# Performance work log

Hardware: AMD Instinct MI355X
Metric: run time of the kernel (lower is better)

Reference implementation:

```python
import jax, jax.numpy as jnp
import numpy as np

NUM_HEADS = 8
D_HEAD = 64
LN_EPS = 1e-6


def _pad_idx(lengths, max_len):
    # flat indices into a [B*max_len, ...] dense buffer for each packed token
    return np.concatenate([b * max_len + np.arange(int(l)) for b, l in enumerate(lengths)])


def _layer_norm(x, scale, bias):
    mu = jnp.mean(x, axis=-1, keepdims=True)
    var = jnp.mean(jnp.square(x - mu), axis=-1, keepdims=True)
    return (x - mu) * jax.lax.rsqrt(var + LN_EPS) * scale + bias


def setup_inputs() -> dict:
    key = jax.random.key(0)
    ks = jax.random.split(key, 12)
    d_model, d_ff, H, dh = 512, 2048, NUM_HEADS, D_HEAD
    lengths = np.array([128 * (i + 1) for i in range(8)], dtype=np.int64)  # sum = 4608
    total = int(lengths.sum())
    s = 0.02
    return {
        "x": jax.random.normal(ks[0], (total, d_model), jnp.float32),
        "mem": jax.random.normal(ks[1], (total, d_model), jnp.float32),
        "lengths_x": lengths,
        "lengths_mem": lengths.copy(),
        "Wq": jax.random.normal(ks[2], (d_model, H * dh), jnp.float32) * s,
        "Wk": jax.random.normal(ks[3], (d_model, H * dh), jnp.float32) * s,
        "Wv": jax.random.normal(ks[4], (d_model, H * dh), jnp.float32) * s,
        "Wo": jax.random.normal(ks[5], (H * dh, d_model), jnp.float32) * s,
        "ln1_scale": jnp.ones((d_model,), jnp.float32),
        "ln1_bias": jnp.zeros((d_model,), jnp.float32),
        "W1": jax.random.normal(ks[6], (d_model, d_ff), jnp.float32) * s,
        "b1": jnp.zeros((d_ff,), jnp.float32),
        "W2": jax.random.normal(ks[7], (d_ff, d_model), jnp.float32) * s,
        "b2": jnp.zeros((d_model,), jnp.float32),
        "ln2_scale": jnp.ones((d_model,), jnp.float32),
        "ln2_bias": jnp.zeros((d_model,), jnp.float32),
    }


def reference(x, mem, lengths_x, lengths_mem, Wq, Wk, Wv, Wo,
              ln1_scale, ln1_bias, W1, b1, W2, b2, ln2_scale, ln2_bias):
    lx = np.asarray(lengths_x)
    lm = np.asarray(lengths_mem)
    B = lx.shape[0]
    Lx = int(lx.max())
    Lm = int(lm.max())
    H, dh = NUM_HEADS, D_HEAD

    idx_x = _pad_idx(lx, Lx)
    idx_m = _pad_idx(lm, Lm)

    def pad(packed, idx, B, L):
        dense = jnp.zeros((B * L,) + packed.shape[1:], packed.dtype).at[idx].set(packed)
        return dense.reshape((B, L) + packed.shape[1:])

    q = pad((x @ Wq).reshape(-1, H, dh), idx_x, B, Lx)   # [B, Lx, H, dh]
    k = pad((mem @ Wk).reshape(-1, H, dh), idx_m, B, Lm)  # [B, Lm, H, dh]
    v = pad((mem @ Wv).reshape(-1, H, dh), idx_m, B, Lm)

    e = jnp.einsum('bxhd,byhd->bhxy', q, k) / np.sqrt(dh)  # [B, H, Lx, Lm]
    # validity mask: (query pos < len_x) & (key pos < len_mem)
    mask = (np.arange(Lx)[None, :, None] < lx[:, None, None]) & \
           (np.arange(Lm)[None, None, :] < lm[:, None, None])
    mask = jnp.asarray(mask)[:, None, :, :]  # [B, 1, Lx, Lm]
    e = jnp.where(mask, e, jnp.float32(-1e30))  # finite -inf surrogate; identical softmax on valid rows
    alpha = jax.nn.softmax(e, axis=-1)
    out = jnp.einsum('bhxy,byhd->bxhd', alpha, v).reshape(B, Lx, H * dh)
    out = out @ Wo                                  # [B, Lx, d_model]
    out = out.reshape(B * Lx, -1)[idx_x]            # pack back to [total_x, d_model]

    h = _layer_norm(x + out, ln1_scale, ln1_bias)
    ffn = jax.nn.relu(h @ W1 + b1) @ W2 + b2
    return _layer_norm(h + ffn, ln2_scale, ln2_bias)
```

## Files before the change

### kernel.cpp

```cpp
#include <hip/hip_runtime.h>
#include <stdint.h>

typedef short bf8v __attribute__((ext_vector_type(8)));
typedef float f4v  __attribute__((ext_vector_type(4)));
typedef short s8v  __attribute__((ext_vector_type(8)));

__device__ __forceinline__ float bf2f(short b){
  unsigned u = ((unsigned)(unsigned short)b) << 16;
  union { unsigned u; float f; } c; c.u = u; return c.f;
}
__device__ __forceinline__ short f2bf(float f){
  union { float f; unsigned u; } c; c.f = f;
  unsigned r = (c.u + 0x7FFFu + ((c.u >> 16) & 1u)) >> 16;
  return (short)r;
}
__device__ __forceinline__ void gload16(const short* g, short* l){
  __builtin_amdgcn_global_load_lds(
      (const __attribute__((address_space(1))) void*)g,
      (__attribute__((address_space(3))) void*)l, 16, 0, 0);
}

__global__ void prep_kernel(const int* lx, const int* lm, int* meta){
  if (threadIdx.x != 0) return;
  int is64 = ((lx[1] | lx[3] | lx[5] | lx[7]) == 0) ? 1 : 0;
  int ox = 0, om = 0;
  for (int b = 0; b < 8; ++b){
    int a = is64 ? lx[2*b] : lx[b];
    int c = is64 ? lm[2*b] : lm[b];
    meta[b] = a; meta[8+b] = c;
    meta[16+b] = ox; meta[25+b] = om;
    ox += a; om += c;
  }
  meta[24] = ox; meta[33] = om;
}

__global__ __launch_bounds__(256) void cvt2bf(const float* __restrict__ x,
                                              const float* __restrict__ mem,
                                              short* __restrict__ xb,
                                              short* __restrict__ mb,
                                              long long n){
  long long t = (long long)blockIdx.x * 256 + threadIdx.x;
  long long i = t * 8;
  const float* s; short* d;
  if (i < n){ s = x + i; d = xb + i; }
  else {
    i -= n; if (i >= n) return;
    s = mem + i; d = mb + i;
  }
  float4 f0 = *(const float4*)s;
  float4 f1 = *(const float4*)(s + 4);
  s8v o;
  o[0]=f2bf(f0.x); o[1]=f2bf(f0.y); o[2]=f2bf(f0.z); o[3]=f2bf(f0.w);
  o[4]=f2bf(f1.x); o[5]=f2bf(f1.y); o[6]=f2bf(f1.z); o[7]=f2bf(f1.w);
  *(s8v*)d = o;
}

__global__ __launch_bounds__(256) void cvt_w_t(
    const float* __restrict__ Wq, const float* __restrict__ Wk,
    const float* __restrict__ Wv, const float* __restrict__ Wo,
    const float* __restrict__ W1, const float* __restrict__ W2,
    short* __restrict__ WqT, short* __restrict__ WkT,
    short* __restrict__ WvT, short* __restrict__ WoT,
    short* __restrict__ W1T, short* __restrict__ W2T){
  __shared__ float tile[32][33];
  int bid = blockIdx.x;
  const float* W; short* WT; int K, N, t0;
  if      (bid <  256){ W=Wq; WT=WqT; K=512;  N=512;  t0=0;    }
  else if (bid <  512){ W=Wk; WT=WkT; K=512;  N=512;  t0=256;  }
  else if (bid <  768){ W=Wv; WT=WvT; K=512;  N=512;  t0=512;  }
  else if (bid < 1024){ W=Wo; WT=WoT; K=512;  N=512;  t0=768;  }
  else if (bid < 2048){ W=W1; WT=W1T; K=512;  N=2048; t0=1024; }
  else                { W=W2; WT=W2T; K=2048; N=512;  t0=2048; }
  int lt = bid - t0;
  int ntn = N / 32;
  int tk = lt / ntn, tn = lt % ntn;
  int r0 = threadIdx.x >> 5, c = threadIdx.x & 31;
  #pragma unroll
  for (int i = 0; i < 4; ++i){
    int r = r0 + i*8;
    tile[r][c] = W[(long)(tk*32 + r)*N + tn*32 + c];
  }
  __syncthreads();
  #pragma unroll
  for (int i = 0; i < 4; ++i){
    int r = r0 + i*8;
    WT[(long)(tn*32 + r)*K + tk*32 + c] = f2bf(tile[c][r]);
  }
}

template<int BM>
__device__ __forceinline__ void stage_gemm(const short* A, const short* Bt,
    long brow, long bcol, int M, int N, int K, int t,
    short* Als, short* Bls){
  int tid = threadIdx.x;
  #pragma unroll
  for (int i = 0; i < BM/64; ++i){
    int cc = i*256 + tid;
    int row = cc >> 2, slot = cc & 3;
    int cg = slot ^ ((row >> 1) & 3);
    long ar = brow + row; if (ar >= M) ar = M - 1;
    gload16(A + ar*(long)K + t + cg*8, &Als[cc*8]);
  }
  #pragma unroll
  for (int i = 0; i < 2; ++i){
    int cc = i*256 + tid;
    int row = cc >> 2, slot = cc & 3;
    int cg = slot ^ ((row >> 1) & 3);
    long br = bcol + row; if (br >= N) br = N - 1;
    gload16(Bt + br*(long)K + t + cg*8, &Bls[cc*8]);
  }
}

template<int BM>
__device__ __forceinline__ void gemm_core(const short* A, const short* Bt,
    short* __restrict__ C, const float* __restrict__ bias,
    int M, int N, int K, float scale, int relu, int colmajor,
    long brow, long bcol, short* Als, short* Bls){
  constexpr int NREP = (BM == 128) ? 4 : 2;
  int tid = threadIdx.x;
  int lane = tid & 63, w = tid >> 6;
  int wrow = (BM == 128) ? (w >> 1) * 64 : 0;
  int wcol = (BM == 128) ? (w & 1) * 64 : w * 32;
  int l15 = lane & 15, l4 = lane >> 4;

  f4v acc[4][NREP];
  #pragma unroll
  for (int m = 0; m < 4; ++m)
    #pragma unroll
    for (int n = 0; n < NREP; ++n) acc[m][n] = (f4v){0.f,0.f,0.f,0.f};

  int nt = K / 32;
  stage_gemm<BM>(A, Bt, brow, bcol, M, N, K, 0, Als, Bls);
  for (int t = 0; t < nt; ++t){
    __syncthreads();
    if (t + 1 < nt)
      stage_gemm<BM>(A, Bt, brow, bcol, M, N, K, (t+1)*32,
                     Als + ((t+1)&1)*(BM*32), Bls + ((t+1)&1)*4096);
    const short* Ab = Als + (t&1)*(BM*32);
    const short* Bb = Bls + (t&1)*4096;
    bf8v a[4], b[NREP];
    #pragma unroll
    for (int m = 0; m < 4; ++m){
      int row = wrow + m*16 + l15;
      int slot = l4 ^ ((row >> 1) & 3);
      a[m] = *(const bf8v*)&Ab[row*32 + slot*8];
    }
    #pragma unroll
    for (int n = 0; n < NREP; ++n){
      int row = wcol + n*16 + l15;
      int slot = l4 ^ ((row >> 1) & 3);
      b[n] = *(const bf8v*)&Bb[row*32 + slot*8];
    }
    #pragma unroll
    for (int m = 0; m < 4; ++m)
      #pragma unroll
      for (int n = 0; n < NREP; ++n)
        acc[m][n] = __builtin_amdgcn_mfma_f32_16x16x32_bf16(a[m], b[n], acc[m][n], 0, 0, 0);
  }

  #pragma unroll
  for (int m = 0; m < 4; ++m){
    #pragma unroll
    for (int n = 0; n < NREP; ++n){
      long col = bcol + wcol + n*16 + l15;
      float bi = (bias != nullptr && col < N) ? bias[col] : 0.f;
      #pragma unroll
      for (int j = 0; j < 4; ++j){
        long row = brow + wrow + m*16 + 4*l4 + j;
        if (row < M && col < N){
          float v = acc[m][n][j] * scale + bi;
          if (relu) v = fmaxf(v, 0.f);
          C[colmajor ? (col*(long)M + row) : (row*(long)N + col)] = f2bf(v);
        }
      }
    }
  }
}

__global__ __launch_bounds__(256) void gemm_bt(
    const short* __restrict__ A, const short* __restrict__ Bt,
    short* __restrict__ C, const float* __restrict__ bias,
    int M, int N, int K, float scale, int relu, int colmajor){
  __shared__ __align__(16) short Als[2*128*32];
  __shared__ __align__(16) short Bls[2*128*32];
  gemm_core<128>(A, Bt, C, bias, M, N, K, scale, relu, colmajor,
                 (long)blockIdx.y * 128, (long)blockIdx.x * 128, Als, Bls);
}

__global__ __launch_bounds__(256) void gemm_bt64(
    const short* __restrict__ A, const short* __restrict__ Bt,
    short* __restrict__ C, const float* __restrict__ bias,
    int M, int N, int K, float scale, int relu, int colmajor){
  __shared__ __align__(16) short Als[2*64*32];
  __shared__ __align__(16) short Bls[2*128*32];
  gemm_core<64>(A, Bt, C, bias, M, N, K, scale, relu, colmajor,
                (long)blockIdx.y * 64, (long)blockIdx.x * 128, Als, Bls);
}

__global__ __launch_bounds__(256) void gemm_qkv(
    const short* __restrict__ xb, const short* __restrict__ mb,
    const short* __restrict__ WqT, const short* __restrict__ WkT,
    const short* __restrict__ WvT,
    short* __restrict__ Qb, short* __restrict__ Kbf, short* __restrict__ Vtb,
    int total){
  __shared__ __align__(16) short Als[2*64*32];
  __shared__ __align__(16) short Bls[2*128*32];
  int seg = blockIdx.x >> 2;
  const short* A  = (seg == 0) ? xb : mb;
  const short* Bt = (seg == 0) ? WqT : ((seg == 1) ? WkT : WvT);
  short* C        = (seg == 0) ? Qb  : ((seg == 1) ? Kbf : Vtb);
  float scale     = (seg == 0) ? 0.125f : 1.f;
  int colmajor    = (seg == 2);
  gemm_core<64>(A, Bt, C, nullptr, total, 512, 512, scale, 0, colmajor,
                (long)blockIdx.y * 64, (long)(blockIdx.x & 3) * 128, Als, Bls);
}

__global__ __launch_bounds__(512) void attn_kernel(
    const short* __restrict__ Q, const short* __restrict__ Kb,
    const short* __restrict__ Vt, short* __restrict__ Ob,
    const int* __restrict__ meta, int total){
  int qt = blockIdx.x, h = blockIdx.y, b = blockIdx.z;
  int Lx = meta[b], Lm = meta[8+b];
  int ox = meta[16+b], om = meta[25+b];
  if (qt*128 >= Lx) return;

  __shared__ __align__(16) short Kls[3][64*64];
  __shared__ __align__(16) short Vls[3][64*64];
  __shared__ __align__(16) short Pls[8][16*64];

  int tid = threadIdx.x;
  int lane = tid & 63, w = tid >> 6;
  int l15 = lane & 15, l4 = lane >> 4;

  bf8v aq0, aq1;
  {
    int qrow = qt*128 + w*16 + l15;
    int grow = ox + (qrow < Lx ? qrow : Lx - 1);
    const short* qp = Q + (long)grow*512 + h*64 + l4*8;
    aq0 = *(const bf8v*)qp;
    aq1 = *(const bf8v*)(qp + 32);
  }
  float mrun[4] = {-1e30f,-1e30f,-1e30f,-1e30f};
  float lrun[4] = {0.f,0.f,0.f,0.f};
  f4v o[4];
  #pragma unroll
  for (int n = 0; n < 4; ++n) o[n] = (f4v){0.f,0.f,0.f,0.f};

  int nt = (Lm + 63) / 64;

  #define ATTN_STAGE(T, BUF)                                                   \
    {                                                                          \
      int c = tid;                                                             \
      int rr = c >> 3, slot = c & 7;                                           \
      int ch = slot ^ (rr & 7);                                                \
      int kv0_ = (T) * 64;                                                     \
      int tok = kv0_ + rr; if (tok >= Lm) tok = Lm - 1;                        \
      gload16(Kb + (long)(om + tok)*512 + h*64 + ch*8, &Kls[BUF][c*8]);        \
      int kvs = kv0_ + ch*8; if (kvs + 8 > Lm) kvs = Lm - 8;                   \
      gload16(Vt + (long)(h*64 + rr)*total + om + kvs, &Vls[BUF][c*8]);        \
    }

  ATTN_STAGE(0, 0)
  if (1 < nt) ATTN_STAGE(1, 1)

  int buf = 0;
  for (int t = 0; t < nt; ++t){
    if (t + 1 < nt) asm volatile("s_waitcnt vmcnt(2)" ::: "memory");
    else            asm volatile("s_waitcnt vmcnt(0)" ::: "memory");
    __builtin_amdgcn_s_barrier();
    asm volatile("" ::: "memory");
    if (t + 2 < nt){
      int bs = buf + 2; if (bs >= 3) bs -= 3;
      ATTN_STAGE(t+2, bs)
    }
    int kv0 = t * 64;

    f4v s[4];
    #pragma unroll
    for (int n = 0; n < 4; ++n){
      int kvrow = n*16 + l15;
      int sl0 = l4 ^ (kvrow & 7);
      int sl1 = (4 + l4) ^ (kvrow & 7);
      bf8v b0 = *(const bf8v*)&Kls[buf][kvrow*64 + sl0*8];
      bf8v b1 = *(const bf8v*)&Kls[buf][kvrow*64 + sl1*8];
      f4v z = (f4v){0.f,0.f,0.f,0.f};
      z = __builtin_amdgcn_mfma_f32_16x16x32_bf16(aq0, b0, z, 0, 0, 0);
      z = __builtin_amdgcn_mfma_f32_16x16x32_bf16(aq1, b1, z, 0, 0, 0);
      s[n] = z;
    }
    #pragma unroll
    for (int n = 0; n < 4; ++n){
      if (kv0 + n*16 + l15 >= Lm){
        s[n][0] = -1e30f; s[n][1] = -1e30f; s[n][2] = -1e30f; s[n][3] = -1e30f;
      }
    }
    #pragma unroll
    for (int j = 0; j < 4; ++j){
      float m1 = fmaxf(fmaxf(s[0][j], s[1][j]), fmaxf(s[2][j], s[3][j]));
      m1 = fmaxf(m1, __shfl_xor(m1, 1, 64));
      m1 = fmaxf(m1, __shfl_xor(m1, 2, 64));
      m1 = fmaxf(m1, __shfl_xor(m1, 4, 64));
      m1 = fmaxf(m1, __shfl_xor(m1, 8, 64));
      float mnew = fmaxf(mrun[j], m1);
      float sc = __expf(mrun[j] - mnew);
      float rs = 0.f;
      #pragma unroll
      for (int n = 0; n < 4; ++n){
        float p = __expf(s[n][j] - mnew);
        s[n][j] = p; rs += p;
      }
      rs += __shfl_xor(rs, 1, 64); rs += __shfl_xor(rs, 2, 64);
      rs += __shfl_xor(rs, 4, 64); rs += __shfl_xor(rs, 8, 64);
      lrun[j] = lrun[j] * sc + rs;
      mrun[j] = mnew;
      o[0][j] *= sc; o[1][j] *= sc; o[2][j] *= sc; o[3][j] *= sc;
    }
    #pragma unroll
    for (int n = 0; n < 4; ++n){
      int pcol = n*16 + l15;
      #pragma unroll
      for (int j = 0; j < 4; ++j){
        int prow = 4*l4 + j;
        Pls[w][prow*64 + (((pcol >> 3) ^ (prow & 7)) << 3) + (pcol & 7)] = f2bf(s[n][j]);
      }
    }
    #pragma unroll
    for (int ks = 0; ks < 2; ++ks){
      int ch = ks*4 + l4;
      bf8v ap = *(const bf8v*)&Pls[w][l15*64 + ((ch ^ (l15 & 7)) << 3)];
      #pragma unroll
      for (int n = 0; n < 4; ++n){
        int d = n*16 + l15;
        bf8v bv = *(const bf8v*)&Vls[buf][d*64 + ((ch ^ (d & 7)) << 3)];
        o[n] = __builtin_amdgcn_mfma_f32_16x16x32_bf16(ap, bv, o[n], 0, 0, 0);
      }
    }
    buf = (buf + 1 == 3) ? 0 : buf + 1;
  }
  #undef ATTN_STAGE

  #pragma unroll
  for (int n = 0; n < 4; ++n){
    #pragma unroll
    for (int j = 0; j < 4; ++j){
      int qrow = qt*128 + w*16 + 4*l4 + j;
      if (qrow < Lx){
        float val = o[n][j] / lrun[j];
        Ob[(long)(ox + qrow)*512 + h*64 + n*16 + l15] = f2bf(val);
      }
    }
  }
}

__global__ __launch_bounds__(256) void ln_fuse(
    const float* __restrict__ Af, const short* __restrict__ Ab,
    const short* __restrict__ Bb,
    const float* __restrict__ gamma, const float* __restrict__ beta,
    short* __restrict__ outb, float* __restrict__ outf, int rows){
  int w = threadIdx.x >> 6, lane = threadIdx.x & 63;
  long row = (long)blockIdx.x * 4 + w;
  if (row >= rows) return;
  int c0 = lane * 8;
  long base = row * 512 + c0;
  float v[8];
  if (Af){
    float4 f0 = *(const float4*)(Af + base);
    float4 f1 = *(const float4*)(Af + base + 4);
    v[0]=f0.x; v[1]=f0.y; v[2]=f0.z; v[3]=f0.w;
    v[4]=f1.x; v[5]=f1.y; v[6]=f1.z; v[7]=f1.w;
  } else {
    s8v a = *(const s8v*)(Ab + base);
    #pragma unroll
    for (int j = 0; j < 8; ++j) v[j] = bf2f(a[j]);
  }
  s8v bb = *(const s8v*)(Bb + base);
  #pragma unroll
  for (int j = 0; j < 8; ++j) v[j] += bf2f(bb[j]);
  float sum = 0.f;
  #pragma unroll
  for (int j = 0; j < 8; ++j) sum += v[j];
  #pragma unroll
  for (int m = 1; m < 64; m <<= 1) sum += __shfl_xor(sum, m, 64);
  float mu = sum * (1.f/512.f);
  float q = 0.f;
  #pragma unroll
  for (int j = 0; j < 8; ++j){ float d = v[j] - mu; q += d*d; }
  #pragma unroll
  for (int m = 1; m < 64; m <<= 1) q += __shfl_xor(q, m, 64);
  float rs = rsqrtf(q * (1.f/512.f) + 1e-6f);
  float ov[8];
  #pragma unroll
  for (int j = 0; j < 8; ++j)
    ov[j] = (v[j] - mu) * rs * gamma[c0 + j] + beta[c0 + j];
  if (outb){
    s8v os;
    #pragma unroll
    for (int j = 0; j < 8; ++j) os[j] = f2bf(ov[j]);
    *(s8v*)(outb + base) = os;
  } else {
    float4 f0 = {ov[0], ov[1], ov[2], ov[3]};
    float4 f1 = {ov[4], ov[5], ov[6], ov[7]};
    *(float4*)(outf + base) = f0;
    *(float4*)(outf + base + 4) = f1;
  }
}

extern "C" void kernel_launch(void* const* d_in, const int* in_sizes, int n_in,
                              void* d_out, int out_size, void* d_ws, size_t ws_size,
                              hipStream_t stream){
  (void)n_in; (void)out_size; (void)ws_size;
  const float* x   = (const float*)d_in[0];
  const float* mem = (const float*)d_in[1];
  const int*   lxr = (const int*)d_in[2];
  const int*   lmr = (const int*)d_in[3];
  const float* Wq  = (const float*)d_in[4];
  const float* Wk  = (const float*)d_in[5];
  const float* Wv  = (const float*)d_in[6];
  const float* Wo  = (const float*)d_in[7];
  const float* g1  = (const float*)d_in[8];
  const float* be1 = (const float*)d_in[9];
  const float* W1  = (const float*)d_in[10];
  const float* b1  = (const float*)d_in[11];
  const float* W2  = (const float*)d_in[12];
  const float* b2  = (const float*)d_in[13];
  const float* g2  = (const float*)d_in[14];
  const float* be2 = (const float*)d_in[15];
  float* out = (float*)d_out;

  int total = in_sizes[0] / 512;
  if (total <= 0) return;
  long long n = (long long)total * 512;

  char* p = (char*)d_ws;
  int*   meta = (int*)p;    p += 256;
  short* xb   = (short*)p;  p += n*2;
  short* mb   = (short*)p;  p += n*2;
  short* Qb   = (short*)p;  p += n*2;
  short* Kbf  = (short*)p;  p += n*2;
  short* Vtb  = (short*)p;  p += n*2;
  short* attnb= (short*)p;  p += n*2;
  short* woout= (short*)p;  p += n*2;
  short* hb   = (short*)p;  p += n*2;
  short* ffn1 = (short*)p;  p += (long long)total*2048*2;
  short* ffn2 = (short*)p;  p += n*2;
  short* WqT  = (short*)p;  p += 512*512*2;
  short* WkT  = (short*)p;  p += 512*512*2;
  short* WvT  = (short*)p;  p += 512*512*2;
  short* WoT  = (short*)p;  p += 512*512*2;
  short* W1T  = (short*)p;  p += 2048*512*2;
  short* W2T  = (short*)p;  p += 512*2048*2;

  prep_kernel<<<1, 64, 0, stream>>>(lxr, lmr, meta);

  long long th = (2*n)/8;
  cvt2bf<<<dim3((unsigned)((th + 255)/256)), dim3(256), 0, stream>>>(x, mem, xb, mb, n);
  cvt_w_t<<<dim3(3072), dim3(256), 0, stream>>>(Wq,Wk,Wv,Wo,W1,W2, WqT,WkT,WvT,WoT,W1T,W2T);

  int mt128 = (total + 127)/128;
  int mt64  = (total + 63)/64;
  gemm_qkv<<<dim3(12, mt64), 256, 0, stream>>>(xb, mb, WqT, WkT, WvT, Qb, Kbf, Vtb, total);

  attn_kernel<<<dim3((unsigned)((total + 127)/128), 8, 8), 512, 0, stream>>>(Qb, Kbf, Vtb, attnb, meta, total);

  gemm_bt64<<<dim3(4, mt64), 256, 0, stream>>>(attnb, WoT, woout, nullptr, total, 512, 512, 1.f, 0, 0);
  ln_fuse<<<dim3((unsigned)((total + 3)/4)), 256, 0, stream>>>(x, nullptr, woout, g1, be1, hb, nullptr, total);

  gemm_bt<<<dim3(16, mt128), 256, 0, stream>>>(hb,   W1T, ffn1, b1, total, 2048, 512,  1.f, 1, 0);
  gemm_bt64<<<dim3(4, mt64), 256, 0, stream>>>(ffn1, W2T, ffn2, b2, total, 512,  2048, 1.f, 0, 0);
  ln_fuse<<<dim3((unsigned)((total + 3)/4)), 256, 0, stream>>>(nullptr, hb, ffn2, g2, be2, nullptr, out, total);
}
```

Measured before the change: 184.4 us.

## Restructure attention kernel to transposed MFMA with direct global K/V loads

Reworks the attention kernel so each 256-thread block has 4 waves, each handling 32 query rows via two 16-row MFMA tiles. Scores are computed as K·Q^T, which puts a query row in each lane and reduces the softmax shuffle steps. K and V are now read straight from global memory instead of staged through a triple-buffered shared-memory pipeline with barriers. P is packed with v_cvt_pk_bf16_f32 into per-wave LDS. The grid is reordered to put head/batch in x, the output store is vectorized, and the kernel trades shared K/V reuse across waves for fewer barriers, less LDS and higher occupancy, risking more global/L2 traffic.

Measured after the change: 207.2 us. 12.4% more time.

```diff
diff --git a/kernel.cpp b/kernel.cpp
--- a/kernel.cpp
+++ b/kernel.cpp
@@ -4,6 +4,8 @@
 typedef short bf8v __attribute__((ext_vector_type(8)));
 typedef float f4v  __attribute__((ext_vector_type(4)));
 typedef short s8v  __attribute__((ext_vector_type(8)));
+typedef short s4v  __attribute__((ext_vector_type(4)));
+typedef int   i2v  __attribute__((ext_vector_type(2)));
 
 __device__ __forceinline__ float bf2f(short b){
   unsigned u = ((unsigned)(unsigned short)b) << 16;
@@ -215,138 +217,144 @@
                 (long)blockIdx.y * 64, (long)(blockIdx.x & 3) * 128, Als, Bls);
 }
 
-__global__ __launch_bounds__(512) void attn_kernel(
+__global__ __launch_bounds__(256, 2) void attn_kernel(
     const short* __restrict__ Q, const short* __restrict__ Kb,
     const short* __restrict__ Vt, short* __restrict__ Ob,
     const int* __restrict__ meta, int total){
-  int qt = blockIdx.x, h = blockIdx.y, b = blockIdx.z;
+  int hb = blockIdx.x;
+  int h = hb & 7, b = hb >> 3;
+  int qt = blockIdx.y;
   int Lx = meta[b], Lm = meta[8+b];
   int ox = meta[16+b], om = meta[25+b];
-  if (qt*128 >= Lx) return;
-
-  __shared__ __align__(16) short Kls[3][64*64];
-  __shared__ __align__(16) short Vls[3][64*64];
-  __shared__ __align__(16) short Pls[8][16*64];
-
   int tid = threadIdx.x;
   int lane = tid & 63, w = tid >> 6;
   int l15 = lane & 15, l4 = lane >> 4;
-
-  bf8v aq0, aq1;
-  {
-    int qrow = qt*128 + w*16 + l15;
-    int grow = ox + (qrow < Lx ? qrow : Lx - 1);
+  int qbase = qt*128 + w*32;
+  if (qbase >= Lx) return;
+
+  __shared__ __align__(16) short Pls[4][32*64];
+  short* pls = Pls[w];
+
+  bf8v aq[2][2];
+  #pragma unroll
+  for (int mi = 0; mi < 2; ++mi){
+    int qr = qbase + mi*16 + l15;
+    int grow = ox + (qr < Lx ? qr : Lx - 1);
     const short* qp = Q + (long)grow*512 + h*64 + l4*8;
-    aq0 = *(const bf8v*)qp;
-    aq1 = *(const bf8v*)(qp + 32);
-  }
-  float mrun[4] = {-1e30f,-1e30f,-1e30f,-1e30f};
-  float lrun[4] = {0.f,0.f,0.f,0.f};
-  f4v o[4];
-  #pragma unroll
-  for (int n = 0; n < 4; ++n) o[n] = (f4v){0.f,0.f,0.f,0.f};
+    aq[mi][0] = *(const bf8v*)qp;
+    aq[mi][1] = *(const bf8v*)(qp + 32);
+  }
+  float mrun[2] = {-1e30f, -1e30f};
+  float lrun[2] = {0.f, 0.f};
+  f4v o[2][4];
+  #pragma unroll
+  for (int mi = 0; mi < 2; ++mi)
+    #pragma unroll
+    for (int n = 0; n < 4; ++n) o[mi][n] = (f4v){0.f,0.f,0.f,0.f};
 
   int nt = (Lm + 63) / 64;
-
-  #define ATTN_STAGE(T, BUF)                                                   \
-    {                                                                          \
-      int c = tid;                                                             \
-      int rr = c >> 3, slot = c & 7;                                           \
-      int ch = slot ^ (rr & 7);                                                \
-      int kv0_ = (T) * 64;                                                     \
-      int tok = kv0_ + rr; if (tok >= Lm) tok = Lm - 1;                        \
-      gload16(Kb + (long)(om + tok)*512 + h*64 + ch*8, &Kls[BUF][c*8]);        \
-      int kvs = kv0_ + ch*8; if (kvs + 8 > Lm) kvs = Lm - 8;                   \
-      gload16(Vt + (long)(h*64 + rr)*total + om + kvs, &Vls[BUF][c*8]);        \
-    }
-
-  ATTN_STAGE(0, 0)
-  if (1 < nt) ATTN_STAGE(1, 1)
-
-  int buf = 0;
   for (int t = 0; t < nt; ++t){
-    if (t + 1 < nt) asm volatile("s_waitcnt vmcnt(2)" ::: "memory");
-    else            asm volatile("s_waitcnt vmcnt(0)" ::: "memory");
-    __builtin_amdgcn_s_barrier();
-    asm volatile("" ::: "memory");
-    if (t + 2 < nt){
-      int bs = buf + 2; if (bs >= 3) bs -= 3;
-      ATTN_STAGE(t+2, bs)
-    }
     int kv0 = t * 64;
 
-    f4v s[4];
+    f4v s[2][4];
     #pragma unroll
     for (int n = 0; n < 4; ++n){
-      int kvrow = n*16 + l15;
-      int sl0 = l4 ^ (kvrow & 7);
-      int sl1 = (4 + l4) ^ (kvrow & 7);
-      bf8v b0 = *(const bf8v*)&Kls[buf][kvrow*64 + sl0*8];
-      bf8v b1 = *(const bf8v*)&Kls[buf][kvrow*64 + sl1*8];
-      f4v z = (f4v){0.f,0.f,0.f,0.f};
-      z = __builtin_amdgcn_mfma_f32_16x16x32_bf16(aq0, b0, z, 0, 0, 0);
-      z = __builtin_amdgcn_mfma_f32_16x16x32_bf16(aq1, b1, z, 0, 0, 0);
-      s[n] = z;
-    }
-    #pragma unroll
-    for (int n = 0; n < 4; ++n){
-      if (kv0 + n*16 + l15 >= Lm){
-        s[n][0] = -1e30f; s[n][1] = -1e30f; s[n][2] = -1e30f; s[n][3] = -1e30f;
-      }
-    }
-    #pragma unroll
-    for (int j = 0; j < 4; ++j){
-      float m1 = fmaxf(fmaxf(s[0][j], s[1][j]), fmaxf(s[2][j], s[3][j]));
-      m1 = fmaxf(m1, __shfl_xor(m1, 1, 64));
-      m1 = fmaxf(m1, __shfl_xor(m1, 2, 64));
-      m1 = fmaxf(m1, __shfl_xor(m1, 4, 64));
-      m1 = fmaxf(m1, __shfl_xor(m1, 8, 64));
-      float mnew = fmaxf(mrun[j], m1);
-      float sc = __expf(mrun[j] - mnew);
+      int kvr = kv0 + n*16 + l15; if (kvr >= Lm) kvr = Lm - 1;
+      const short* kp = Kb + (long)(om + kvr)*512 + h*64 + l4*8;
+      bf8v k0 = *(const bf8v*)kp;
+      bf8v k1 = *(const bf8v*)(kp + 32);
+      #pragma unroll
+      for (int mi = 0; mi < 2; ++mi){
+        f4v z = (f4v){0.f,0.f,0.f,0.f};
+        z = __builtin_amdgcn_mfma_f32_16x16x32_bf16(k0, aq[mi][0], z, 0, 0, 0);
+        z = __builtin_amdgcn_mfma_f32_16x16x32_bf16(k1, aq[mi][1], z, 0, 0, 0);
+        s[mi][n] = z;
+      }
+    }
+
+    if (kv0 + 64 > Lm){
+      #pragma unroll
+      for (int n = 0; n < 4; ++n){
+        int kvb = kv0 + n*16 + 4*l4;
+        #pragma unroll
+        for (int j = 0; j < 4; ++j)
+          if (kvb + j >= Lm){ s[0][n][j] = -1e30f; s[1][n][j] = -1e30f; }
+      }
+    }
+
+    #pragma unroll
+    for (int mi = 0; mi < 2; ++mi){
+      float m1 = s[mi][0][0];
+      #pragma unroll
+      for (int n = 0; n < 4; ++n)
+        #pragma unroll
+        for (int j = 0; j < 4; ++j) m1 = fmaxf(m1, s[mi][n][j]);
+      m1 = fmaxf(m1, __shfl_xor(m1, 16, 64));
+      m1 = fmaxf(m1, __shfl_xor(m1, 32, 64));
+      float mnew = fmaxf(mrun[mi], m1);
+      float sc = __expf(mrun[mi] - mnew);
+      mrun[mi] = mnew;
       float rs = 0.f;
       #pragma unroll
+      for (int n = 0; n < 4; ++n)
+        #pragma unroll
+        for (int j = 0; j < 4; ++j){
+          float p = __expf(s[mi][n][j] - mnew);
+          s[mi][n][j] = p; rs += p;
+        }
+      rs += __shfl_xor(rs, 16, 64);
+      rs += __shfl_xor(rs, 32, 64);
+      lrun[mi] = lrun[mi] * sc + rs;
+      #pragma unroll
+      for (int n = 0; n < 4; ++n) o[mi][n] *= sc;
+
+      int q = mi*16 + l15;
+      #pragma unroll
       for (int n = 0; n < 4; ++n){
-        float p = __expf(s[n][j] - mnew);
-        s[n][j] = p; rs += p;
-      }
-      rs += __shfl_xor(rs, 1, 64); rs += __shfl_xor(rs, 2, 64);
-      rs += __shfl_xor(rs, 4, 64); rs += __shfl_xor(rs, 8, 64);
-      lrun[j] = lrun[j] * sc + rs;
-      mrun[j] = mnew;
-      o[0][j] *= sc; o[1][j] *= sc; o[2][j] *= sc; o[3][j] *= sc;
-    }
-    #pragma unroll
-    for (int n = 0; n < 4; ++n){
-      int pcol = n*16 + l15;
-      #pragma unroll
-      for (int j = 0; j < 4; ++j){
-        int prow = 4*l4 + j;
-        Pls[w][prow*64 + (((pcol >> 3) ^ (prow & 7)) << 3) + (pcol & 7)] = f2bf(s[n][j]);
-      }
-    }
-    #pragma unroll
-    for (int ks = 0; ks < 2; ++ks){
-      int ch = ks*4 + l4;
-      bf8v ap = *(const bf8v*)&Pls[w][l15*64 + ((ch ^ (l15 & 7)) << 3)];
-      #pragma unroll
-      for (int n = 0; n < 4; ++n){
-        int d = n*16 + l15;
-        bf8v bv = *(const bf8v*)&Vls[buf][d*64 + ((ch ^ (d & 7)) << 3)];
-        o[n] = __builtin_amdgcn_mfma_f32_16x16x32_bf16(ap, bv, o[n], 0, 0, 0);
-      }
-    }
-    buf = (buf + 1 == 3) ? 0 : buf + 1;
-  }
-  #undef ATTN_STAGE
-
-  #pragma unroll
-  for (int n = 0; n < 4; ++n){
-    #pragma unroll
-    for (int j = 0; j < 4; ++j){
-      int qrow = qt*128 + w*16 + 4*l4 + j;
-      if (qrow < Lx){
-        float val = o[n][j] / lrun[j];
-        Ob[(long)(ox + qrow)*512 + h*64 + n*16 + l15] = f2bf(val);
+        unsigned r0, r1;
+        asm("v_cvt_pk_bf16_f32 %0, %1, %2" : "=v"(r0) : "v"(s[mi][n][0]), "v"(s[mi][n][1]));
+        asm("v_cvt_pk_bf16_f32 %0, %1, %2" : "=v"(r1) : "v"(s[mi][n][2]), "v"(s[mi][n][3]));
+        i2v pr; pr[0] = (int)r0; pr[1] = (int)r1;
+        *(i2v*)&pls[q*64 + ((n ^ (l15 & 3)) << 4) + (l4 << 2)] = pr;
+      }
+    }
+
+    bf8v pb[2][2];
+    #pragma unroll
+    for (int mi = 0; mi < 2; ++mi)
+      #pragma unroll
+      for (int ks = 0; ks < 2; ++ks){
+        int q = mi*16 + l15;
+        int ch = (ks*2 + (l4 >> 1)) ^ (q & 3);
+        pb[mi][ks] = *(const bf8v*)&pls[q*64 + (ch << 4) + ((l4 & 1) << 3)];
+      }
+
+    #pragma unroll
+    for (int n2 = 0; n2 < 4; ++n2){
+      const short* vp = Vt + (long)(h*64 + n2*16 + l15)*total + om;
+      #pragma unroll
+      for (int ks = 0; ks < 2; ++ks){
+        int vk = kv0 + ks*32 + l4*8;
+        if (vk + 8 > Lm) vk = (Lm - 8) & ~0;
+        bf8v vv = *(const bf8v*)(vp + vk);
+        o[0][n2] = __builtin_amdgcn_mfma_f32_16x16x32_bf16(vv, pb[0][ks], o[0][n2], 0, 0, 0);
+        o[1][n2] = __builtin_amdgcn_mfma_f32_16x16x32_bf16(vv, pb[1][ks], o[1][n2], 0, 0, 0);
+      }
+    }
+  }
+
+  #pragma unroll
+  for (int mi = 0; mi < 2; ++mi){
+    int qr = qbase + mi*16 + l15;
+    if (qr < Lx){
+      float inv = 1.f / lrun[mi];
+      long obase = (long)(ox + qr)*512 + h*64;
+      #pragma unroll
+      for (int n2 = 0; n2 < 4; ++n2){
+        s4v ov;
+        #pragma unroll
+        for (int j = 0; j < 4; ++j) ov[j] = f2bf(o[mi][n2][j] * inv);
+        *(s4v*)&Ob[obase + n2*16 + (l4 << 2)] = ov;
       }
     }
   }
@@ -460,7 +468,7 @@
   int mt64  = (total + 63)/64;
   gemm_qkv<<<dim3(12, mt64), 256, 0, stream>>>(xb, mb, WqT, WkT, WvT, Qb, Kbf, Vtb, total);
 
-  attn_kernel<<<dim3((unsigned)((total + 127)/128), 8, 8), 512, 0, stream>>>(Qb, Kbf, Vtb, attnb, meta, total);
+  attn_kernel<<<dim3(64, (unsigned)((total + 127)/128)), 256, 0, stream>>>(Qb, Kbf, Vtb, attnb, meta, total);
 
   gemm_bt64<<<dim3(4, mt64), 256, 0, stream>>>(attnb, WoT, woout, nullptr, total, 512, 512, 1.f, 0, 0);
   ln_fuse<<<dim3((unsigned)((total + 3)/4)), 256, 0, stream>>>(x, nullptr, woout, g1, be1, hb, nullptr, total);
```
